# Optimization experiments

Hardware: AMD Instinct MI355X
Metric: run time of the kernel (lower is better)

Reference implementation:

```python
import jax, jax.numpy as jnp
import numpy as np

TEMPERATURE = 0.1
THR = 0.2
BORDER_RM = 2


def setup_inputs() -> dict:
    key = jax.random.key(0)
    k0, k1 = jax.random.split(key)
    N, L, S, C = 2, 4800, 4800, 256
    return {
        "feat_c0": jax.random.normal(k0, (N, L, C), dtype=jnp.float32),
        "feat_c1": jax.random.normal(k1, (N, S, C), dtype=jnp.float32),
        "h0c": 60, "w0c": 80, "h1c": 60, "w1c": 80,
    }


def _border_valid(h, w, bd):
    # Faithful to torch mask_border: only the FIRST `bd` rows/cols are masked
    # (the negative slices m[:, -bd:0] in the source are empty no-ops).
    vh = jnp.arange(h) >= bd
    vw = jnp.arange(w) >= bd
    return (vh[:, None] & vw[None, :]).reshape(-1)  # [h*w]


def reference(feat_c0, feat_c1, h0c, w0c, h1c, w1c):
    C = feat_c0.shape[-1]
    scale = 1.0 / (C ** 0.5)  # 'sqrt_feat_dim' feature normalizer
    f0 = feat_c0 * scale
    f1 = feat_c1 * scale

    # dual-softmax confidence matrix [N, L, S]
    sim = jnp.einsum("nlc,nsc->nls", f0, f1) / TEMPERATURE
    conf = jax.nn.softmax(sim, axis=1) * jax.nn.softmax(sim, axis=2)

    # threshold + border removal (no padding masks in data)
    mask = conf > THR
    valid0 = _border_valid(h0c, w0c, BORDER_RM)  # [L]
    valid1 = _border_valid(h1c, w1c, BORDER_RM)  # [S]
    mask = mask & valid0[None, :, None] & valid1[None, None, :]

    # mutual nearest neighbour filtering
    mask = mask & (conf == conf.max(axis=2, keepdims=True)) \
                & (conf == conf.max(axis=1, keepdims=True))

    # match extraction (JIT-friendly padded form):
    # j_ids[b, i] = column of the (unique) True in row i; match_mask marks valid rows.
    j_ids = jnp.argmax(mask, axis=2)               # [N, L] int
    match_mask = jnp.any(mask, axis=2)             # [N, L] bool
    mconf = jnp.take_along_axis(conf, j_ids[..., None], axis=2)[..., 0]
    mconf = jnp.where(match_mask, mconf, 0.0)      # [N, L]

    return conf, match_mask, j_ids, mconf
```

## Files before the change

kernel.cpp:

```cpp
#include <hip/hip_runtime.h>


#define Ncst 2
#define Lc 4800
#define Sc 4800
#define Cc 256
#define KA 512
#define KB 256
#define LP 4864
#define THRC 0.2f

typedef float f32x4 __attribute__((ext_vector_type(4)));
typedef _Float16 f16x8 __attribute__((ext_vector_type(8)));

#define AS1(p) ((__attribute__((address_space(1))) void*)(p))
#define AS3(p) ((__attribute__((address_space(3))) void*)(p))

__global__ __launch_bounds__(256) void convert_kernel(
    const float* __restrict__ f0, const float* __restrict__ f1,
    unsigned short* __restrict__ A2, unsigned short* __restrict__ B2,
    float* __restrict__ rs, float* __restrict__ cs)
{
    int idx = blockIdx.x * 256 + threadIdx.x;
    if (idx < Ncst * Lc) { rs[idx] = 0.f; cs[idx] = 0.f; }
    if (idx >= Ncst * LP * (Cc / 8)) return;
    int k8  = idx & (Cc / 8 - 1);
    int row = (idx >> 5) % LP;
    int n   = idx / (LP * (Cc / 8));

    float av[8], bv[8];
    if (row < Lc) {
        const float4* pa = (const float4*)(f0 + ((size_t)n * Lc + row) * Cc + k8 * 8);
        float4 a0 = pa[0], a1 = pa[1];
        av[0]=a0.x; av[1]=a0.y; av[2]=a0.z; av[3]=a0.w;
        av[4]=a1.x; av[5]=a1.y; av[6]=a1.z; av[7]=a1.w;
        const float4* pb = (const float4*)(f1 + ((size_t)n * Sc + row) * Cc + k8 * 8);
        float4 b0 = pb[0], b1 = pb[1];
        bv[0]=b0.x; bv[1]=b0.y; bv[2]=b0.z; bv[3]=b0.w;
        bv[4]=b1.x; bv[5]=b1.y; bv[6]=b1.z; bv[7]=b1.w;
    } else {
        for (int i = 0; i < 8; ++i) { av[i] = 0.f; bv[i] = 0.f; }
    }

    _Float16 ahi[8], alo[8], bhi[8];
#pragma unroll
    for (int i = 0; i < 8; ++i) {
        _Float16 h = (_Float16)av[i];
        ahi[i] = h;
        alo[i] = (_Float16)(av[i] - (float)h);
        bhi[i] = (_Float16)bv[i];
    }
    size_t abase = ((size_t)n * LP + row) * KA + k8 * 8;
    size_t bbase = ((size_t)n * LP + row) * KB + k8 * 8;
    *(uint4*)&A2[abase]       = *(uint4*)ahi;
    *(uint4*)&A2[abase + 256] = *(uint4*)alo;
    *(uint4*)&B2[bbase]       = *(uint4*)bhi;
}

template <int DUMMY>
__global__ __launch_bounds__(256, 3) void gemm_kernel(
    const unsigned short* __restrict__ A2, const unsigned short* __restrict__ B2,
    float* __restrict__ eout, float* __restrict__ rs, float* __restrict__ cs)
{
    __shared__ __attribute__((aligned(16))) unsigned short lds[2][1536 * 8];

    int flat = blockIdx.x + 38 * blockIdx.y + 1444 * blockIdx.z;
    int m    = (flat & 7) * 361 + (flat >> 3);
    const int tn = m % 38;
    const int tm = (m / 38) % 38;
    const int n  = m / 1444;

    const int tid  = threadIdx.x;
    const int wave = tid >> 6;
    const int lane = tid & 63;
    const int wm   = wave >> 1;
    const int wn   = wave & 1;
    const int ml   = lane & 15;
    const int kq   = lane >> 4;

    const unsigned short* Ab = A2 + ((size_t)n * LP + (size_t)tm * 128) * KA;
    const unsigned short* Bb = B2 + ((size_t)n * LP + (size_t)tn * 128) * KB;

    const unsigned short* gsrc[6];
    int gdst[6];
#pragma unroll
    for (int c = 0; c < 6; ++c) {
        int reg = c >> 1;
        int s   = (c & 1) * 256 + tid;
        int row = s >> 2;
        int q   = (s & 3) ^ ((row >> 1) & 3);
        if (reg == 0)      gsrc[c] = Ab + (size_t)row * KA + q * 8;
        else if (reg == 1) gsrc[c] = Ab + (size_t)row * KA + 256 + q * 8;
        else               gsrc[c] = Bb + (size_t)row * KB + q * 8;
        gdst[c] = (reg * 512 + s) * 8;
    }

    int aoff[4], boff[4];
#pragma unroll
    for (int i = 0; i < 4; ++i) {
        int ar = wm * 64 + i * 16 + ml;
        aoff[i] = (ar * 4 + (kq ^ ((ar >> 1) & 3))) * 8;
        int br = wn * 64 + i * 16 + ml;
        boff[i] = (br * 4 + (kq ^ ((br >> 1) & 3))) * 8;
    }

#define STAGE(bb, tt) do { _Pragma("unroll") for (int c_ = 0; c_ < 6; ++c_) \
    __builtin_amdgcn_global_load_lds(AS1(gsrc[c_] + (tt) * 32), AS3(&lds[bb][gdst[c_]]), 16, 0, 0); } while (0)

    f32x4 acc[4][4] = {};

    STAGE(0, 0);
    __syncthreads();

#pragma unroll
    for (int t = 0; t < 8; ++t) {
        const int b = t & 1;
        if (t < 7) STAGE(b ^ 1, t + 1);
        f16x8 ah[4], al[4], bf_[4];
#pragma unroll
        for (int i = 0; i < 4; ++i) {
            ah[i]  = *(const f16x8*)&lds[b][aoff[i]];
            al[i]  = *(const f16x8*)&lds[b][4096 + aoff[i]];
            bf_[i] = *(const f16x8*)&lds[b][8192 + boff[i]];
        }
#pragma unroll
        for (int i = 0; i < 4; ++i)
#pragma unroll
            for (int j = 0; j < 4; ++j) {
                acc[i][j] = __builtin_amdgcn_mfma_f32_16x16x32_f16(ah[i], bf_[j], acc[i][j], 0, 0, 0);
                acc[i][j] = __builtin_amdgcn_mfma_f32_16x16x32_f16(al[i], bf_[j], acc[i][j], 0, 0, 0);
            }
        __syncthreads();
    }
#undef STAGE

    const float alpha = 5.0f / 128.0f;
#pragma unroll
    for (int i = 0; i < 4; ++i) {
#pragma unroll
        for (int r = 0; r < 4; ++r) {
            int gl = tm * 128 + wm * 64 + i * 16 + kq * 4 + r;
            bool rok = gl < Lc;
#pragma unroll
            for (int j = 0; j < 4; ++j) {
                int gs = tn * 128 + wn * 64 + j * 16 + ml;
                bool ok = rok && (gs < Sc);
                float ev = ok ? __expf(acc[i][j][r] * alpha) : 0.f;
                acc[i][j][r] = ev;
                if (ok) eout[((size_t)n * Lc + gl) * Sc + gs] = ev;
            }
        }
    }
#pragma unroll
    for (int i = 0; i < 4; ++i) {
#pragma unroll
        for (int r = 0; r < 4; ++r) {
            float rp = acc[i][0][r] + acc[i][1][r] + acc[i][2][r] + acc[i][3][r];
            rp += __shfl_xor(rp, 1);
            rp += __shfl_xor(rp, 2);
            rp += __shfl_xor(rp, 4);
            rp += __shfl_xor(rp, 8);
            int gl = tm * 128 + wm * 64 + i * 16 + kq * 4 + r;
            if (ml == 0 && gl < Lc) atomicAdd(&rs[(size_t)n * Lc + gl], rp);
        }
    }
#pragma unroll
    for (int j = 0; j < 4; ++j) {
        float cp = 0.f;
#pragma unroll
        for (int i = 0; i < 4; ++i)
#pragma unroll
            for (int r = 0; r < 4; ++r) cp += acc[i][j][r];
        cp += __shfl_xor(cp, 16);
        cp += __shfl_xor(cp, 32);
        int gs = tn * 128 + wn * 64 + j * 16 + ml;
        if (kq == 0 && gs < Sc) atomicAdd(&cs[(size_t)n * Sc + gs], cp);
    }
}

__global__ __launch_bounds__(256) void inv_kernel(
    const float* __restrict__ cs, float* __restrict__ csinv)
{
    int i = blockIdx.x * 256 + threadIdx.x;
    if (i < Ncst * Lc) csinv[i] = 1.0f / cs[i];
}

__global__ __launch_bounds__(256) void conf_kernel(
    float* __restrict__ confio,
    const float* __restrict__ rs, const float* __restrict__ csinv,
    float* __restrict__ rcm)
{
    __shared__ float sw[4];
    int b = blockIdx.x;
    int n = b / Lc;
    f32x4* row = (f32x4*)(confio + (size_t)b * Sc);
    const f32x4* civ = (const f32x4*)(csinv + (size_t)n * Sc);
    int tid = threadIdx.x;
    float riv = 1.0f / rs[b];
    float lmax = 0.f;
    for (int v = tid; v < Sc / 4; v += 256) {
        f32x4 e4 = row[v];
        f32x4 c4 = civ[v];
        f32x4 o  = e4 * e4 * riv * c4;
        __builtin_nontemporal_store(o, &row[v]);
        lmax = fmaxf(lmax, fmaxf(fmaxf(o.x, o.y), fmaxf(o.z, o.w)));
    }
#pragma unroll
    for (int off = 1; off < 64; off <<= 1) lmax = fmaxf(lmax, __shfl_xor(lmax, off));
    if ((tid & 63) == 0) sw[tid >> 6] = lmax;
    __syncthreads();
    if (tid == 0) rcm[b] = fmaxf(fmaxf(sw[0], sw[1]), fmaxf(sw[2], sw[3]));
}

__global__ __launch_bounds__(256) void finalize_kernel(
    const float* __restrict__ conf, const float* __restrict__ rcm,
    const int* __restrict__ h0p, const int* __restrict__ w0p,
    const int* __restrict__ h1p, const int* __restrict__ w1p,
    float* __restrict__ out_match, float* __restrict__ out_j, float* __restrict__ out_mconf)
{
    int i = blockIdx.x * 256 + threadIdx.x;
    if (i >= Ncst * Lc) return;
    int n = i / Lc, l = i % Lc;
    float mm = rcm[i];
    float fm = 0.f, fj = 0.f, fc = 0.f;
    if (mm > THRC) {
        int w0 = *w0p, w1 = *w1p;
        if ((l / w0) >= 2 && (l % w0) >= 2) {
            const float* rowp = conf + ((size_t)n * Lc + l) * Sc;
            for (int s = 0; s < Sc; ++s) {
                float c = rowp[s];
                if (c == mm && (s / w1) >= 2 && (s % w1) >= 2) {
                    bool ismax = true;
                    const float* colp = conf + (size_t)n * Lc * Sc + s;
                    for (int lp = 0; lp < Lc; ++lp) {
                        if (colp[(size_t)lp * Sc] > c) { ismax = false; break; }
                    }
                    if (ismax) { fm = 1.f; fj = (float)s; fc = c; break; }
                }
            }
        }
    }
    out_match[i] = fm; out_j[i] = fj; out_mconf[i] = fc;
}

extern "C" void kernel_launch(void* const* d_in, const int* in_sizes, int n_in,
                              void* d_out, int out_size, void* d_ws, size_t ws_size,
                              hipStream_t stream) {
    const float* f0 = (const float*)d_in[0];
    const float* f1 = (const float*)d_in[1];
    const int* h0p = (const int*)d_in[2];
    const int* w0p = (const int*)d_in[3];
    const int* h1p = (const int*)d_in[4];
    const int* w1p = (const int*)d_in[5];

    char* ws = (char*)d_ws;
    unsigned short* A2 = (unsigned short*)ws;
    unsigned short* B2 = (unsigned short*)(ws + 9961472);
    float* rs    = (float*)(ws + 14942208);
    float* cs    = (float*)(ws + 14980608);
    float* csinv = (float*)(ws + 15019008);
    float* rcm   = (float*)(ws + 15057408);

    float* conf      = (float*)d_out;
    float* out_match = conf + (size_t)Ncst * Lc * Sc;
    float* out_j     = out_match + Ncst * Lc;
    float* out_mconf = out_j + Ncst * Lc;

    convert_kernel<<<(Ncst * LP * (Cc / 8) + 255) / 256, 256, 0, stream>>>(
        f0, f1, A2, B2, rs, cs);

    dim3 gg(38, 38, Ncst);
    gemm_kernel<0><<<gg, 256, 0, stream>>>(A2, B2, conf, rs, cs);

    inv_kernel<<<(Ncst * Lc + 255) / 256, 256, 0, stream>>>(cs, csinv);

    conf_kernel<<<Ncst * Lc, 256, 0, stream>>>(conf, rs, csinv, rcm);

    finalize_kernel<<<(Ncst * Lc + 255) / 256, 256, 0, stream>>>(
        conf, rcm, h0p, w0p, h1p, w1p, out_match, out_j, out_mconf);
}
```

Baseline: 317.0 us.

## Stage GEMM exp tile through LDS for coalesced vector stores; drop inv kernel

The GEMM epilogue no longer writes exp values with scattered scalar stores straight from MFMA register layout. It stages each half of the 128x128 tile in LDS (padded stride 132) and writes rows as coalesced float4 stores. The separate column-reciprocal kernel is also removed, and conf_kernel computes 1/cs inline. This trades extra LDS traffic and barriers, plus redundant divides in conf_kernel, for better global write coalescing on the large 184MB exp output and one fewer launch.

```diff
diff --git a/kernel.cpp b/kernel.cpp
--- a/kernel.cpp
+++ b/kernel.cpp
@@ -136,7 +136,7 @@
 
     const float alpha = 5.0f / 128.0f;
 #pragma unroll
-    for (int i = 0; i < 4; ++i) {
+    for (int i = 0; i < 4; ++i)
 #pragma unroll
         for (int r = 0; r < 4; ++r) {
             int gl = tm * 128 + wm * 64 + i * 16 + kq * 4 + r;
@@ -145,14 +145,11 @@
             for (int j = 0; j < 4; ++j) {
                 int gs = tn * 128 + wn * 64 + j * 16 + ml;
                 bool ok = rok && (gs < Sc);
-                float ev = ok ? __expf(acc[i][j][r] * alpha) : 0.f;
-                acc[i][j][r] = ev;
-                if (ok) eout[((size_t)n * Lc + gl) * Sc + gs] = ev;
-            }
-        }
-    }
-#pragma unroll
-    for (int i = 0; i < 4; ++i) {
+                acc[i][j][r] = ok ? __expf(acc[i][j][r] * alpha) : 0.f;
+            }
+        }
+#pragma unroll
+    for (int i = 0; i < 4; ++i)
 #pragma unroll
         for (int r = 0; r < 4; ++r) {
             float rp = acc[i][0][r] + acc[i][1][r] + acc[i][2][r] + acc[i][3][r];
@@ -163,7 +160,6 @@
             int gl = tm * 128 + wm * 64 + i * 16 + kq * 4 + r;
             if (ml == 0 && gl < Lc) atomicAdd(&rs[(size_t)n * Lc + gl], rp);
         }
-    }
 #pragma unroll
     for (int j = 0; j < 4; ++j) {
         float cp = 0.f;
@@ -176,32 +172,60 @@
         int gs = tn * 128 + wn * 64 + j * 16 + ml;
         if (kq == 0 && gs < Sc) atomicAdd(&cs[(size_t)n * Sc + gs], cp);
     }
-}
-
-__global__ __launch_bounds__(256) void inv_kernel(
-    const float* __restrict__ cs, float* __restrict__ csinv)
-{
-    int i = blockIdx.x * 256 + threadIdx.x;
-    if (i < Ncst * Lc) csinv[i] = 1.0f / cs[i];
+
+    float* tb = (float*)&lds[0][0];
+    const int CS = 132;
+#pragma unroll
+    for (int p = 0; p < 2; ++p) {
+        __syncthreads();
+#pragma unroll
+        for (int ih = 0; ih < 2; ++ih) {
+            int i   = 2 * p + ih;
+            int lr0 = wm * 32 + ih * 16 + kq * 4;
+#pragma unroll
+            for (int j = 0; j < 4; ++j) {
+                int col = wn * 64 + j * 16 + ml;
+#pragma unroll
+                for (int r = 0; r < 4; ++r)
+                    tb[(lr0 + r) * CS + col] = acc[i][j][r];
+            }
+        }
+        __syncthreads();
+#pragma unroll
+        for (int u = 0; u < 8; ++u) {
+            int idx = u * 256 + tid;
+            int lr  = idx >> 5;
+            int cv  = idx & 31;
+            int grow = tm * 128 + (lr >> 5) * 64 + (2 * p + ((lr >> 4) & 1)) * 16 + (lr & 15);
+            int gcol = tn * 128 + cv * 4;
+            if (grow < Lc && gcol + 3 < Sc) {
+                f32x4 v = *(const f32x4*)&tb[lr * CS + cv * 4];
+                *(f32x4*)&eout[((size_t)n * Lc + grow) * Sc + gcol] = v;
+            }
+        }
+    }
 }
 
 __global__ __launch_bounds__(256) void conf_kernel(
     float* __restrict__ confio,
-    const float* __restrict__ rs, const float* __restrict__ csinv,
+    const float* __restrict__ rs, const float* __restrict__ cs,
     float* __restrict__ rcm)
 {
     __shared__ float sw[4];
     int b = blockIdx.x;
     int n = b / Lc;
     f32x4* row = (f32x4*)(confio + (size_t)b * Sc);
-    const f32x4* civ = (const f32x4*)(csinv + (size_t)n * Sc);
+    const f32x4* csv = (const f32x4*)(cs + (size_t)n * Sc);
     int tid = threadIdx.x;
     float riv = 1.0f / rs[b];
     float lmax = 0.f;
     for (int v = tid; v < Sc / 4; v += 256) {
         f32x4 e4 = row[v];
-        f32x4 c4 = civ[v];
-        f32x4 o  = e4 * e4 * riv * c4;
+        f32x4 c4 = csv[v];
+        f32x4 civ4;
+        civ4.x = 1.0f / c4.x; civ4.y = 1.0f / c4.y;
+        civ4.z = 1.0f / c4.z; civ4.w = 1.0f / c4.w;
+        f32x4 o = e4 * e4 * riv * civ4;
         __builtin_nontemporal_store(o, &row[v]);
         lmax = fmaxf(lmax, fmaxf(fmaxf(o.x, o.y), fmaxf(o.z, o.w)));
     }
@@ -256,10 +280,9 @@
     char* ws = (char*)d_ws;
     unsigned short* A2 = (unsigned short*)ws;
     unsigned short* B2 = (unsigned short*)(ws + 9961472);
-    float* rs    = (float*)(ws + 14942208);
-    float* cs    = (float*)(ws + 14980608);
-    float* csinv = (float*)(ws + 15019008);
-    float* rcm   = (float*)(ws + 15057408);
+    float* rs  = (float*)(ws + 14942208);
+    float* cs  = (float*)(ws + 14980608);
+    float* rcm = (float*)(ws + 15019008);
 
     float* conf      = (float*)d_out;
     float* out_match = conf + (size_t)Ncst * Lc * Sc;
@@ -272,9 +295,7 @@
     dim3 gg(38, 38, Ncst);
     gemm_kernel<0><<<gg, 256, 0, stream>>>(A2, B2, conf, rs, cs);
 
-    inv_kernel<<<(Ncst * Lc + 255) / 256, 256, 0, stream>>>(cs, csinv);
-
-    conf_kernel<<<Ncst * Lc, 256, 0, stream>>>(conf, rs, csinv, rcm);
+    conf_kernel<<<Ncst * Lc, 256, 0, stream>>>(conf, rs, cs, rcm);
 
     finalize_kernel<<<(Ncst * Lc + 255) / 256, 256, 0, stream>>>(
         conf, rcm, h0p, w0p, h1p, w1p, out_match, out_j, out_mconf);
```

Result: no change. 319.3 us (+0.7%).
